# Kernel tuning notes

Hardware: AMD Instinct MI355X
Metric: run time of the kernel (lower is better)

Reference implementation:

```python
import math
import jax, jax.numpy as jnp
import numpy as np

NUM_BUCKETS = 32
MAX_DISTANCE = 128
N_HEADS = 16
D_KV = 64


def _relative_position_bucket(relative_position, num_buckets=NUM_BUCKETS, max_distance=MAX_DISTANCE):
    # bidirectional (encoder) version, faithful to T5Attention._relative_position_bucket
    nb = num_buckets // 2
    rel_buckets = (relative_position > 0).astype(jnp.int32) * nb
    rp = jnp.abs(relative_position)
    max_exact = nb // 2
    is_small = rp < max_exact
    # log-spaced buckets for large distances; clamp arg of log to >=1 to avoid -inf
    rp_large = max_exact + (
        jnp.log(jnp.maximum(rp, 1).astype(jnp.float32) / max_exact)
        / math.log(max_distance / max_exact)
        * (nb - max_exact)
    ).astype(jnp.int32)
    rp_large = jnp.minimum(rp_large, nb - 1)
    return rel_buckets + jnp.where(is_small, rp, rp_large)


def setup_inputs() -> dict:
    key = jax.random.key(0)
    ks = jax.random.split(key, 6)
    B, S, D = 2, 2048, 1024
    scale = 0.02
    return {
        "hidden_states": jax.random.normal(ks[0], (B, S, D), dtype=jnp.float32),
        "Wq": jax.random.normal(ks[1], (D, N_HEADS * D_KV), dtype=jnp.float32) * scale,
        "Wk": jax.random.normal(ks[2], (D, N_HEADS * D_KV), dtype=jnp.float32) * scale,
        "Wv": jax.random.normal(ks[3], (D, N_HEADS * D_KV), dtype=jnp.float32) * scale,
        "Wo": jax.random.normal(ks[4], (N_HEADS * D_KV, D), dtype=jnp.float32) * scale,
        "rel_bias": jax.random.normal(ks[5], (NUM_BUCKETS, N_HEADS), dtype=jnp.float32),
    }


def reference(hidden_states, Wq, Wk, Wv, Wo, rel_bias):
    B, S, D = hidden_states.shape
    H, dk = N_HEADS, D_KV
    q = (hidden_states @ Wq).reshape(B, S, H, dk)
    k = (hidden_states @ Wk).reshape(B, S, H, dk)
    v = (hidden_states @ Wv).reshape(B, S, H, dk)

    pos = jnp.arange(S)
    relative_position = pos[None, :] - pos[:, None]          # [S_q, S_k]
    buckets = _relative_position_bucket(relative_position)    # [S_q, S_k]
    bias = rel_bias[buckets].transpose(2, 0, 1)               # [H, S_q, S_k]

    # T5 attention: NO 1/sqrt(d) scaling
    scores = jnp.einsum('bqhd,bkhd->bhqk', q, k) + bias[None]
    attn = jax.nn.softmax(scores, axis=-1)
    ctx = jnp.einsum('bhqk,bkhd->bqhd', attn, v).reshape(B, S, H * dk)
    return ctx @ Wo
```

## Files before the change

kernel.cpp:

```cpp
#include <hip/hip_runtime.h>
#include <hip/hip_bf16.h>
#include <stdint.h>

#define S_LEN 2048
#define NH 16
#define NB_DELTA (2*S_LEN-1)
#define PST 72
#define LOG2E 1.4426950408889634f

typedef __attribute__((ext_vector_type(8))) __bf16 bf16x8;
typedef __attribute__((ext_vector_type(4))) float f32x4;

__device__ __forceinline__ unsigned short f2bf(float f){
    union { float f; unsigned int u; } v; v.f = f;
    unsigned int u = v.u;
    return (unsigned short)((u + 0x7FFFu + ((u >> 16) & 1u)) >> 16);
}
__device__ __forceinline__ float bf2f(unsigned short u){
    union { unsigned int u; float f; } v; v.u = ((unsigned int)u) << 16;
    return v.f;
}
__device__ __forceinline__ unsigned int pkbf(float a, float b){
    __hip_bfloat162 h = __float22bfloat162_rn(float2{a, b});
    unsigned int u;
    __builtin_memcpy(&u, &h, 4);
    return u;
}
#if __has_builtin(__builtin_amdgcn_exp2f)
__device__ __forceinline__ float fexp2(float x){ return __builtin_amdgcn_exp2f(x); }
#else
__device__ __forceinline__ float fexp2(float x){ return __expf(x * 0.69314718056f); }
#endif

__device__ __forceinline__ void gload16(const void* g, void* l){
    __builtin_amdgcn_global_load_lds(
        (const __attribute__((address_space(1))) void*)(uintptr_t)g,
        (__attribute__((address_space(3))) void*)(uintptr_t)l, 16, 0, 0);
}

__global__ __launch_bounds__(256) void prep_kernel(
    const float* __restrict__ hs, unsigned short* __restrict__ hsb,
    const float* __restrict__ W0, const float* __restrict__ W1,
    const float* __restrict__ W2, const float* __restrict__ W3,
    unsigned short* __restrict__ D0, unsigned short* __restrict__ D1,
    unsigned short* __restrict__ D2, unsigned short* __restrict__ D3,
    const float* __restrict__ rel_bias, float* __restrict__ biasT){
    if (blockIdx.z == 4) {
        int bi = blockIdx.y * 32 + blockIdx.x;
        for (int it = 0; it < 4; it++) {
            int i = bi * 4096 + it * 1024 + threadIdx.x * 4;
            float4 f = *(const float4*)(hs + i);
            ushort4 o;
            o.x = f2bf(f.x); o.y = f2bf(f.y); o.z = f2bf(f.z); o.w = f2bf(f.w);
            *(ushort4*)(hsb + i) = o;
        }
        if (bi < 16) {
            int t = bi * 256 + threadIdx.x;
            if (t < NB_DELTA) {
                int delta = t - (S_LEN - 1);
                int bucket = (delta > 0) ? 16 : 0;
                int a = delta < 0 ? -delta : delta;
                int b;
                if (a < 8) b = a;
                else {
                    int bl = 33 - __builtin_clz(a * a);
                    b = bl < 15 ? bl : 15;
                }
                bucket += b;
                for (int h = 0; h < NH; h++)
                    biasT[h * NB_DELTA + t] = rel_bias[bucket * NH + h];
            }
        }
        return;
    }
    const float* src; unsigned short* dst;
    switch (blockIdx.z) {
        case 0: src = W0; dst = D0; break;
        case 1: src = W1; dst = D1; break;
        case 2: src = W2; dst = D2; break;
        default: src = W3; dst = D3; break;
    }
    __shared__ float tile[32][33];
    int bx = blockIdx.x, by = blockIdx.y;
    int tx = threadIdx.x & 31, ty = threadIdx.x >> 5;
    for (int i = 0; i < 4; i++)
        tile[ty + 8*i][tx] = src[(size_t)(by*32 + ty + 8*i) * 1024 + bx*32 + tx];
    __syncthreads();
    for (int i = 0; i < 4; i++)
        dst[(size_t)(bx*32 + ty + 8*i) * 1024 + by*32 + tx] = f2bf(tile[tx][ty + 8*i]);
}

template<int MODE, int BM>
__global__ __launch_bounds__(256) void gemm_bt_kernel(const unsigned short* __restrict__ A,
                                                      const unsigned short* __restrict__ BT,
                                                      float* __restrict__ C0,
                                                      unsigned short* __restrict__ C1,
                                                      int Kdim, int ldc){
    constexpr int IT = BM / 32;
    __shared__ __align__(16) unsigned short As[BM * 64];
    __shared__ __align__(16) unsigned short Bs[128 * 64];
    const int t = threadIdx.x;
    const int wave = t >> 6, lane = t & 63;
    const int quad = lane >> 4, l16 = lane & 15;
    const int wm = (wave >> 1) * (BM / 2), wn = (wave & 1) * 64;
    const size_t row0 = (size_t)blockIdx.y * BM, col0 = (size_t)blockIdx.x * 128;

    const int srow8 = lane >> 3;
    const int gg = (lane & 7) ^ srow8;
    const unsigned short* gA = A  + (row0 + wave * 8 + srow8) * (size_t)Kdim + gg * 8;
    const unsigned short* gB = BT + (col0 + wave * 8 + srow8) * (size_t)Kdim + gg * 8;

    f32x4 acc[IT][4] = {};

    for (int kt = 0; kt < Kdim; kt += 64) {
        for (int p = 0; p < BM / 32; p++)
            gload16(gA + (size_t)(p * 32) * Kdim + kt, &As[(p * 32 + wave * 8) * 64]);
        for (int p = 0; p < 4; p++)
            gload16(gB + (size_t)(p * 32) * Kdim + kt, &Bs[(p * 32 + wave * 8) * 64]);
        __syncthreads();
        bf16x8 a[2][IT], b[2][4];
        for (int ks = 0; ks < 2; ks++) {
            for (int i = 0; i < IT; i++)
                a[ks][i] = *(const bf16x8*)(&As[(wm + i*16 + l16) * 64 + (((ks*4 + quad) ^ (l16 & 7)) * 8)]);
            for (int j = 0; j < 4; j++)
                b[ks][j] = *(const bf16x8*)(&Bs[(wn + j*16 + l16) * 64 + (((ks*4 + quad) ^ (l16 & 7)) * 8)]);
        }
        for (int ks = 0; ks < 2; ks++)
            for (int i = 0; i < IT; i++)
                for (int j = 0; j < 4; j++)
                    acc[i][j] = __builtin_amdgcn_mfma_f32_16x16x32_bf16(a[ks][i], b[ks][j], acc[i][j], 0, 0, 0);
        __syncthreads();
    }
    for (int i = 0; i < IT; i++)
        for (int j = 0; j < 4; j++) {
            size_t r0 = row0 + wm + i*16 + quad*4;
            size_t c  = col0 + wn + j*16 + l16;
            if (MODE == 0) {
                for (int r = 0; r < 4; r++)
                    C0[(r0 + r) * ldc + c] = acc[i][j][r];
            } else {
                float qs = (c < 1024) ? LOG2E : 1.0f;
                for (int r = 0; r < 4; r++)
                    C1[(r0 + r) * ldc + c] = f2bf(acc[i][j][r] * qs);
            }
        }
}

__global__ __launch_bounds__(256) void vtrans_kernel(const unsigned short* __restrict__ qkv,
                                                     unsigned short* __restrict__ vt){
    __shared__ unsigned short tile[64][72];
    const int v0 = blockIdx.x * 64, s0 = blockIdx.y * 64, b = blockIdx.z;
    const int tx = threadIdx.x & 7, ty = threadIdx.x >> 3;
    for (int i = 0; i < 2; i++)
        *(int4*)&tile[ty + 32*i][tx * 8] =
            *(const int4*)(qkv + (size_t)(b * 2048 + s0 + ty + 32*i) * 3072 + 2048 + v0 + tx * 8);
    __syncthreads();
    for (int i = 0; i < 2; i++) {
        int v = ty + 32*i;
        int sl = tx * 8;
        ushort4 o0, o1;
        o0.x = tile[sl+0][v]; o0.y = tile[sl+1][v]; o0.z = tile[sl+2][v]; o0.w = tile[sl+3][v];
        o1.x = tile[sl+4][v]; o1.y = tile[sl+5][v]; o1.z = tile[sl+6][v]; o1.w = tile[sl+7][v];
        unsigned short* dst = vt + (size_t)(b * 1024 + v0 + v) * 2048 + s0 + sl;
        *(ushort4*)dst = o0; *(ushort4*)(dst + 4) = o1;
    }
}

__global__ __launch_bounds__(256, 4) void flash10_kernel(
    const unsigned short* __restrict__ qkv,
    const unsigned short* __restrict__ vt,
    const float* __restrict__ biasT,
    const float* __restrict__ rel_bias,
    unsigned short* __restrict__ ctxpb,
    float* __restrict__ rsbuf)
{
    const int qt = blockIdx.x, h = blockIdx.y;
    const int b = blockIdx.z >> 1, ck = blockIdx.z & 1;
    const int kt0 = ck << 10;
    const int t = threadIdx.x;
    const int w = t >> 6, lane = t & 63, quad = lane >> 4, l16 = lane & 15;
    const int q0 = qt * 128;

    __shared__ __align__(16) unsigned short Ks[64 * 64];
    __shared__ __align__(16) unsigned short Vs[64 * 64];
    __shared__ __align__(16) unsigned short Pb[128 * PST];
    __shared__ float bias_s[192];

    const float b15 = (rel_bias[15 * NH + h] - 16.f) * LOG2E;
    const float b31 = (rel_bias[31 * NH + h] - 16.f) * LOG2E;

    for (int s = 0; s < 4; s++) {
        int g = t + s * 256;
        int r = g >> 3, c = (g & 7) * 8;
        *(int4*)&Pb[r * PST + c] =
            *(const int4*)(qkv + (size_t)(b * S_LEN + q0 + r) * 3072 + h * 64 + c);
    }
    __syncthreads();
    bf16x8 qb[2][2];
    for (int nt = 0; nt < 2; nt++)
        for (int ks = 0; ks < 2; ks++)
            qb[ks][nt] = *(const bf16x8*)&Pb[(w * 32 + nt * 16 + l16) * PST + ks * 32 + quad * 8];

    float rsum[2] = {0.f, 0.f};
    f32x4 ctx[4][2] = {};

    const float* biasRow = biasT + h * NB_DELTA + 2047;

    const int srow8 = lane >> 3;
    const int gg = (lane & 7) ^ srow8;
    const int swz = ((l16 & 7) * 8);

    for (int kt = kt0; kt < kt0 + 1024; kt += 64) {
        const int off = kt - q0;
        const bool cst = (off >= 255) || (off <= -191);
        __syncthreads();
        {
            const unsigned short* kb = qkv + (size_t)(b * S_LEN + kt + w * 8 + srow8) * 3072 + 1024 + h * 64 + gg * 8;
            const unsigned short* vb = vt + (size_t)(b * 1024 + h * 64 + w * 8 + srow8) * 2048 + kt + gg * 8;
            gload16(kb,                     &Ks[(w * 8) * 64]);
            gload16(kb + (size_t)32 * 3072, &Ks[(32 + w * 8) * 64]);
            gload16(vb,                     &Vs[(w * 8) * 64]);
            gload16(vb + (size_t)32 * 2048, &Vs[(32 + w * 8) * 64]);
            if (!cst && t < 192) bias_s[t] = (biasRow[off - 127 + t] - 16.f) * LOG2E;
        }
        __syncthreads();

        f32x4 st[4][2] = {};
        for (int ks = 0; ks < 2; ks++)
            for (int nb = 0; nb < 4; nb++) {
                bf16x8 ka = *(const bf16x8*)&Ks[(nb * 16 + l16) * 64 + (((ks * 4 + quad) * 8) ^ swz)];
                st[nb][0] = __builtin_amdgcn_mfma_f32_16x16x32_bf16(ka, qb[ks][0], st[nb][0], 0, 0, 0);
                st[nb][1] = __builtin_amdgcn_mfma_f32_16x16x32_bf16(ka, qb[ks][1], st[nb][1], 0, 0, 0);
            }
        const float bc = (off > 0) ? b31 : b15;
        for (int nt = 0; nt < 2; nt++) {
            const int ib = quad * 4 + 127 - w * 32 - nt * 16 - l16;
            float rs = 0.f;
            for (int nb = 0; nb < 4; nb++) {
                float e0, e1, e2, e3;
                if (cst) {
                    e0 = fexp2(st[nb][nt][0] + bc);
                    e1 = fexp2(st[nb][nt][1] + bc);
                    e2 = fexp2(st[nb][nt][2] + bc);
                    e3 = fexp2(st[nb][nt][3] + bc);
                } else {
                    e0 = fexp2(st[nb][nt][0] + bias_s[ib + nb * 16 + 0]);
                    e1 = fexp2(st[nb][nt][1] + bias_s[ib + nb * 16 + 1]);
                    e2 = fexp2(st[nb][nt][2] + bias_s[ib + nb * 16 + 2]);
                    e3 = fexp2(st[nb][nt][3] + bias_s[ib + nb * 16 + 3]);
                }
                rs += (e0 + e1) + (e2 + e3);
                uint2 pk; pk.x = pkbf(e0, e1); pk.y = pkbf(e2, e3);
                *(uint2*)&Pb[(w * 32 + nt * 16 + l16) * PST + nb * 16 + quad * 4] = pk;
            }
            rsum[nt] += rs;
        }
        for (int ks = 0; ks < 2; ks++) {
            bf16x8 pb0 = *(const bf16x8*)&Pb[(w * 32 + l16) * PST + ks * 32 + quad * 8];
            bf16x8 pb1 = *(const bf16x8*)&Pb[(w * 32 + 16 + l16) * PST + ks * 32 + quad * 8];
            for (int nd = 0; nd < 4; nd++) {
                bf16x8 va = *(const bf16x8*)&Vs[(nd * 16 + l16) * 64 + (((ks * 4 + quad) * 8) ^ swz)];
                ctx[nd][0] = __builtin_amdgcn_mfma_f32_16x16x32_bf16(va, pb0, ctx[nd][0], 0, 0, 0);
                ctx[nd][1] = __builtin_amdgcn_mfma_f32_16x16x32_bf16(va, pb1, ctx[nd][1], 0, 0, 0);
            }
        }
    }
    unsigned short* cp = ctxpb + (size_t)ck * 4096 * 1024;
    for (int nt = 0; nt < 2; nt++) {
        float rs = rsum[nt];
        rs += __shfl_xor(rs, 16, 64);
        rs += __shfl_xor(rs, 32, 64);
        int row = b * S_LEN + q0 + w * 32 + nt * 16 + l16;
        if (quad == 0) rsbuf[((size_t)ck * 4096 + row) * 16 + h] = rs;
        for (int nd = 0; nd < 4; nd++) {
            uint2 pk;
            pk.x = pkbf(ctx[nd][nt][0], ctx[nd][nt][1]);
            pk.y = pkbf(ctx[nd][nt][2], ctx[nd][nt][3]);
            *(uint2*)&cp[(size_t)row * 1024 + h * 64 + nd * 16 + quad * 4] = pk;
        }
    }
}

__global__ __launch_bounds__(256) void combine_kernel(const unsigned short* __restrict__ ctxpb,
                                                      const float* __restrict__ rsbuf,
                                                      unsigned short* __restrict__ ctxb){
    int e = blockIdx.x * 256 + threadIdx.x;
    int row = e >> 8;
    int c4 = (e & 255) * 4;
    int h = c4 >> 6;
    float l = rsbuf[(size_t)row * 16 + h] + rsbuf[((size_t)4096 + row) * 16 + h];
    ushort4 a  = *(const ushort4*)&ctxpb[(size_t)row * 1024 + c4];
    ushort4 b2 = *(const ushort4*)&ctxpb[(size_t)4096 * 1024 + (size_t)row * 1024 + c4];
    float inv = 1.f / l;
    uint2 o;
    o.x = pkbf((bf2f(a.x) + bf2f(b2.x)) * inv, (bf2f(a.y) + bf2f(b2.y)) * inv);
    o.y = pkbf((bf2f(a.z) + bf2f(b2.z)) * inv, (bf2f(a.w) + bf2f(b2.w)) * inv);
    *(uint2*)&ctxb[(size_t)row * 1024 + c4] = o;
}

extern "C" void kernel_launch(void* const* d_in, const int* in_sizes, int n_in,
                              void* d_out, int out_size, void* d_ws, size_t ws_size,
                              hipStream_t stream) {
    const float* hs       = (const float*)d_in[0];
    const float* Wq       = (const float*)d_in[1];
    const float* Wk       = (const float*)d_in[2];
    const float* Wv       = (const float*)d_in[3];
    const float* Wo       = (const float*)d_in[4];
    const float* rel_bias = (const float*)d_in[5];
    float* out = (float*)d_out;

    char* ws = (char*)d_ws;
    float* biasT          = (float*)ws;           ws += 262144;
    unsigned short* hsb   = (unsigned short*)ws;  ws += 8388608;
    unsigned short* WT    = (unsigned short*)ws;  ws += 6291456;
    unsigned short* WoT   = (unsigned short*)ws;  ws += 2097152;
    unsigned short* qkvb  = (unsigned short*)ws;  ws += 25165824;
    unsigned short* Vtg   = (unsigned short*)ws;  ws += 8388608;
    unsigned short* ctxb  = (unsigned short*)ws;  ws += 8388608;
    unsigned short* ctxpb = (unsigned short*)ws;  ws += 16777216;
    float* rsbuf          = (float*)ws;

    prep_kernel<<<dim3(32, 32, 5), 256, 0, stream>>>(
        hs, hsb, Wq, Wk, Wv, Wo,
        WT, WT + 1024 * 1024, WT + 2 * 1024 * 1024, WoT, rel_bias, biasT);

    gemm_bt_kernel<1, 64><<<dim3(24, 64), 256, 0, stream>>>(hsb, WT, nullptr, qkvb, 1024, 3072);
    vtrans_kernel<<<dim3(16, 32, 2), 256, 0, stream>>>(qkvb, Vtg);
    flash10_kernel<<<dim3(S_LEN / 128, NH, 4), 256, 0, stream>>>(qkvb, Vtg, biasT, rel_bias, ctxpb, rsbuf);
    combine_kernel<<<4096, 256, 0, stream>>>(ctxpb, rsbuf, ctxb);
    gemm_bt_kernel<0, 64><<<dim3(8, 64), 256, 0, stream>>>(ctxb, WoT, out, nullptr, 1024, 1024);
}
```

Baseline: 203.0 us.

## Fuse V transpose into QKV GEMM epilogue and split-combine into output GEMM

The QKV GEMM now writes Q/K into a narrower buffer and stores V directly transposed, which removes the separate vtrans kernel. The output GEMM loads both split-K partial contexts, normalizes them by the summed row sums and packs bf16 into LDS itself, which removes the combine kernel and the ctxb round trip. This drops two launches and several intermediate buffers. The cost is that the output GEMM's A-tile load becomes synchronous register loads with ALU work in place of async global-to-LDS loads, and the transposed V stores are scattered 8-byte writes.

```diff
diff --git a/kernel.cpp b/kernel.cpp
--- a/kernel.cpp
+++ b/kernel.cpp
@@ -90,84 +90,130 @@
         dst[(size_t)(bx*32 + ty + 8*i) * 1024 + by*32 + tx] = f2bf(tile[tx][ty + 8*i]);
 }
 
-template<int MODE, int BM>
-__global__ __launch_bounds__(256) void gemm_bt_kernel(const unsigned short* __restrict__ A,
-                                                      const unsigned short* __restrict__ BT,
-                                                      float* __restrict__ C0,
-                                                      unsigned short* __restrict__ C1,
-                                                      int Kdim, int ldc){
-    constexpr int IT = BM / 32;
-    __shared__ __align__(16) unsigned short As[BM * 64];
+__global__ __launch_bounds__(256) void gemm_qkv_kernel(const unsigned short* __restrict__ A,
+                                                       const unsigned short* __restrict__ BT,
+                                                       unsigned short* __restrict__ qk,
+                                                       unsigned short* __restrict__ vt){
+    const int Kdim = 1024;
+    __shared__ __align__(16) unsigned short As[64 * 64];
     __shared__ __align__(16) unsigned short Bs[128 * 64];
     const int t = threadIdx.x;
     const int wave = t >> 6, lane = t & 63;
     const int quad = lane >> 4, l16 = lane & 15;
-    const int wm = (wave >> 1) * (BM / 2), wn = (wave & 1) * 64;
-    const size_t row0 = (size_t)blockIdx.y * BM, col0 = (size_t)blockIdx.x * 128;
+    const int wm = (wave >> 1) * 32, wn = (wave & 1) * 64;
+    const size_t row0 = (size_t)blockIdx.y * 64, col0 = (size_t)blockIdx.x * 128;
 
     const int srow8 = lane >> 3;
     const int gg = (lane & 7) ^ srow8;
     const unsigned short* gA = A  + (row0 + wave * 8 + srow8) * (size_t)Kdim + gg * 8;
     const unsigned short* gB = BT + (col0 + wave * 8 + srow8) * (size_t)Kdim + gg * 8;
 
-    f32x4 acc[IT][4] = {};
+    f32x4 acc[2][4] = {};
 
     for (int kt = 0; kt < Kdim; kt += 64) {
-        for (int p = 0; p < BM / 32; p++)
+        for (int p = 0; p < 2; p++)
             gload16(gA + (size_t)(p * 32) * Kdim + kt, &As[(p * 32 + wave * 8) * 64]);
         for (int p = 0; p < 4; p++)
             gload16(gB + (size_t)(p * 32) * Kdim + kt, &Bs[(p * 32 + wave * 8) * 64]);
         __syncthreads();
-        bf16x8 a[2][IT], b[2][4];
+        bf16x8 a[2][2], b[2][4];
         for (int ks = 0; ks < 2; ks++) {
-            for (int i = 0; i < IT; i++)
+            for (int i = 0; i < 2; i++)
                 a[ks][i] = *(const bf16x8*)(&As[(wm + i*16 + l16) * 64 + (((ks*4 + quad) ^ (l16 & 7)) * 8)]);
             for (int j = 0; j < 4; j++)
                 b[ks][j] = *(const bf16x8*)(&Bs[(wn + j*16 + l16) * 64 + (((ks*4 + quad) ^ (l16 & 7)) * 8)]);
         }
         for (int ks = 0; ks < 2; ks++)
-            for (int i = 0; i < IT; i++)
+            for (int i = 0; i < 2; i++)
                 for (int j = 0; j < 4; j++)
                     acc[i][j] = __builtin_amdgcn_mfma_f32_16x16x32_bf16(a[ks][i], b[ks][j], acc[i][j], 0, 0, 0);
         __syncthreads();
     }
-    for (int i = 0; i < IT; i++)
+    for (int i = 0; i < 2; i++)
         for (int j = 0; j < 4; j++) {
             size_t r0 = row0 + wm + i*16 + quad*4;
             size_t c  = col0 + wn + j*16 + l16;
-            if (MODE == 0) {
-                for (int r = 0; r < 4; r++)
-                    C0[(r0 + r) * ldc + c] = acc[i][j][r];
-            } else {
+            if (c < 2048) {
                 float qs = (c < 1024) ? LOG2E : 1.0f;
                 for (int r = 0; r < 4; r++)
-                    C1[(r0 + r) * ldc + c] = f2bf(acc[i][j][r] * qs);
-            }
-        }
-}
-
-__global__ __launch_bounds__(256) void vtrans_kernel(const unsigned short* __restrict__ qkv,
-                                                     unsigned short* __restrict__ vt){
-    __shared__ unsigned short tile[64][72];
-    const int v0 = blockIdx.x * 64, s0 = blockIdx.y * 64, b = blockIdx.z;
-    const int tx = threadIdx.x & 7, ty = threadIdx.x >> 3;
+                    qk[(r0 + r) * 2048 + c] = f2bf(acc[i][j][r] * qs);
+            } else {
+                int bb = (int)(r0 >> 11);
+                int s  = (int)(r0 & 2047);
+                ushort4 pk;
+                pk.x = f2bf(acc[i][j][0]); pk.y = f2bf(acc[i][j][1]);
+                pk.z = f2bf(acc[i][j][2]); pk.w = f2bf(acc[i][j][3]);
+                *(ushort4*)(vt + ((size_t)(bb * 1024) + (c - 2048)) * 2048 + s) = pk;
+            }
+        }
+}
+
+__global__ __launch_bounds__(256) void gemm_out_kernel(const unsigned short* __restrict__ ctxpb,
+                                                       const float* __restrict__ rsbuf,
+                                                       const unsigned short* __restrict__ BT,
+                                                       float* __restrict__ C0){
+    const int Kdim = 1024;
+    __shared__ __align__(16) unsigned short As[64 * 64];
+    __shared__ __align__(16) unsigned short Bs[128 * 64];
+    const int t = threadIdx.x;
+    const int wave = t >> 6, lane = t & 63;
+    const int quad = lane >> 4, l16 = lane & 15;
+    const int wm = (wave >> 1) * 32, wn = (wave & 1) * 64;
+    const size_t row0 = (size_t)blockIdx.y * 64, col0 = (size_t)blockIdx.x * 128;
+
+    const int srow8 = lane >> 3;
+    const int gg = (lane & 7) ^ srow8;
+    const unsigned short* gB = BT + (col0 + wave * 8 + srow8) * (size_t)Kdim + gg * 8;
+    const int arow0 = (int)row0 + wave * 8 + srow8;
+    const int acol  = gg * 8;
+
+    f32x4 acc[2][4] = {};
+
+    for (int kt = 0; kt < Kdim; kt += 64) {
+        for (int p = 0; p < 4; p++)
+            gload16(gB + (size_t)(p * 32) * Kdim + kt, &Bs[(p * 32 + wave * 8) * 64]);
+        const int h = kt >> 6;
+        for (int p = 0; p < 2; p++) {
+            const int r = arow0 + p * 32;
+            uint4 a0 = *(const uint4*)&ctxpb[(size_t)r * 1024 + kt + acol];
+            uint4 a1 = *(const uint4*)&ctxpb[(size_t)4096 * 1024 + (size_t)r * 1024 + kt + acol];
+            float inv = 1.f / (rsbuf[(size_t)r * 16 + h] + rsbuf[((size_t)4096 + r) * 16 + h]);
+            uint4 o;
+            o.x = pkbf((bf2f(a0.x & 0xffff) + bf2f(a1.x & 0xffff)) * inv,
+                       (bf2f(a0.x >> 16)    + bf2f(a1.x >> 16))    * inv);
+            o.y = pkbf((bf2f(a0.y & 0xffff) + bf2f(a1.y & 0xffff)) * inv,
+                       (bf2f(a0.y >> 16)    + bf2f(a1.y >> 16))    * inv);
+            o.z = pkbf((bf2f(a0.z & 0xffff) + bf2f(a1.z & 0xffff)) * inv,
+                       (bf2f(a0.z >> 16)    + bf2f(a1.z >> 16))    * inv);
+            o.w = pkbf((bf2f(a0.w & 0xffff) + bf2f(a1.w & 0xffff)) * inv,
+                       (bf2f(a0.w >> 16)    + bf2f(a1.w >> 16))    * inv);
+            *(uint4*)&As[(p * 32 + wave * 8 + srow8) * 64 + (lane & 7) * 8] = o;
+        }
+        __syncthreads();
+        bf16x8 a[2][2], b[2][4];
+        for (int ks = 0; ks < 2; ks++) {
+            for (int i = 0; i < 2; i++)
+                a[ks][i] = *(const bf16x8*)(&As[(wm + i*16 + l16) * 64 + (((ks*4 + quad) ^ (l16 & 7)) * 8)]);
+            for (int j = 0; j < 4; j++)
+                b[ks][j] = *(const bf16x8*)(&Bs[(wn + j*16 + l16) * 64 + (((ks*4 + quad) ^ (l16 & 7)) * 8)]);
+        }
+        for (int ks = 0; ks < 2; ks++)
+            for (int i = 0; i < 2; i++)
+                for (int j = 0; j < 4; j++)
+                    acc[i][j] = __builtin_amdgcn_mfma_f32_16x16x32_bf16(a[ks][i], b[ks][j], acc[i][j], 0, 0, 0);
+        __syncthreads();
+    }
     for (int i = 0; i < 2; i++)
-        *(int4*)&tile[ty + 32*i][tx * 8] =
-            *(const int4*)(qkv + (size_t)(b * 2048 + s0 + ty + 32*i) * 3072 + 2048 + v0 + tx * 8);
-    __syncthreads();
-    for (int i = 0; i < 2; i++) {
-        int v = ty + 32*i;
-        int sl = tx * 8;
-        ushort4 o0, o1;
-        o0.x = tile[sl+0][v]; o0.y = tile[sl+1][v]; o0.z = tile[sl+2][v]; o0.w = tile[sl+3][v];
-        o1.x = tile[sl+4][v]; o1.y = tile[sl+5][v]; o1.z = tile[sl+6][v]; o1.w = tile[sl+7][v];
-        unsigned short* dst = vt + (size_t)(b * 1024 + v0 + v) * 2048 + s0 + sl;
-        *(ushort4*)dst = o0; *(ushort4*)(dst + 4) = o1;
-    }
+        for (int j = 0; j < 4; j++) {
+            size_t r0 = row0 + wm + i*16 + quad*4;
+            size_t c  = col0 + wn + j*16 + l16;
+            for (int r = 0; r < 4; r++)
+                C0[(r0 + r) * 1024 + c] = acc[i][j][r];
+        }
 }
 
 __global__ __launch_bounds__(256, 4) void flash10_kernel(
-    const unsigned short* __restrict__ qkv,
+    const unsigned short* __restrict__ qk,
     const unsigned short* __restrict__ vt,
     const float* __restrict__ biasT,
     const float* __restrict__ rel_bias,
@@ -193,7 +239,7 @@
         int g = t + s * 256;
         int r = g >> 3, c = (g & 7) * 8;
         *(int4*)&Pb[r * PST + c] =
-            *(const int4*)(qkv + (size_t)(b * S_LEN + q0 + r) * 3072 + h * 64 + c);
+            *(const int4*)(qk + (size_t)(b * S_LEN + q0 + r) * 2048 + h * 64 + c);
     }
     __syncthreads();
     bf16x8 qb[2][2];
@@ -215,10 +261,10 @@
         const bool cst = (off >= 255) || (off <= -191);
         __syncthreads();
         {
-            const unsigned short* kb = qkv + (size_t)(b * S_LEN + kt + w * 8 + srow8) * 3072 + 1024 + h * 64 + gg * 8;
+            const unsigned short* kb = qk + (size_t)(b * S_LEN + kt + w * 8 + srow8) * 2048 + 1024 + h * 64 + gg * 8;
             const unsigned short* vb = vt + (size_t)(b * 1024 + h * 64 + w * 8 + srow8) * 2048 + kt + gg * 8;
             gload16(kb,                     &Ks[(w * 8) * 64]);
-            gload16(kb + (size_t)32 * 3072, &Ks[(32 + w * 8) * 64]);
+            gload16(kb + (size_t)32 * 2048, &Ks[(32 + w * 8) * 64]);
             gload16(vb,                     &Vs[(w * 8) * 64]);
             gload16(vb + (size_t)32 * 2048, &Vs[(32 + w * 8) * 64]);
             if (!cst && t < 192) bias_s[t] = (biasRow[off - 127 + t] - 16.f) * LOG2E;
@@ -281,23 +327,6 @@
     }
 }
 
-__global__ __launch_bounds__(256) void combine_kernel(const unsigned short* __restrict__ ctxpb,
-                                                      const float* __restrict__ rsbuf,
-                                                      unsigned short* __restrict__ ctxb){
-    int e = blockIdx.x * 256 + threadIdx.x;
-    int row = e >> 8;
-    int c4 = (e & 255) * 4;
-    int h = c4 >> 6;
-    float l = rsbuf[(size_t)row * 16 + h] + rsbuf[((size_t)4096 + row) * 16 + h];
-    ushort4 a  = *(const ushort4*)&ctxpb[(size_t)row * 1024 + c4];
-    ushort4 b2 = *(const ushort4*)&ctxpb[(size_t)4096 * 1024 + (size_t)row * 1024 + c4];
-    float inv = 1.f / l;
-    uint2 o;
-    o.x = pkbf((bf2f(a.x) + bf2f(b2.x)) * inv, (bf2f(a.y) + bf2f(b2.y)) * inv);
-    o.y = pkbf((bf2f(a.z) + bf2f(b2.z)) * inv, (bf2f(a.w) + bf2f(b2.w)) * inv);
-    *(uint2*)&ctxb[(size_t)row * 1024 + c4] = o;
-}
-
 extern "C" void kernel_launch(void* const* d_in, const int* in_sizes, int n_in,
                               void* d_out, int out_size, void* d_ws, size_t ws_size,
                               hipStream_t stream) {
@@ -314,9 +343,8 @@
     unsigned short* hsb   = (unsigned short*)ws;  ws += 8388608;
     unsigned short* WT    = (unsigned short*)ws;  ws += 6291456;
     unsigned short* WoT   = (unsigned short*)ws;  ws += 2097152;
-    unsigned short* qkvb  = (unsigned short*)ws;  ws += 25165824;
+    unsigned short* qkbuf = (unsigned short*)ws;  ws += 16777216;
     unsigned short* Vtg   = (unsigned short*)ws;  ws += 8388608;
-    unsigned short* ctxb  = (unsigned short*)ws;  ws += 8388608;
     unsigned short* ctxpb = (unsigned short*)ws;  ws += 16777216;
     float* rsbuf          = (float*)ws;
 
@@ -324,9 +352,7 @@
         hs, hsb, Wq, Wk, Wv, Wo,
         WT, WT + 1024 * 1024, WT + 2 * 1024 * 1024, WoT, rel_bias, biasT);
 
-    gemm_bt_kernel<1, 64><<<dim3(24, 64), 256, 0, stream>>>(hsb, WT, nullptr, qkvb, 1024, 3072);
-    vtrans_kernel<<<dim3(16, 32, 2), 256, 0, stream>>>(qkvb, Vtg);
-    flash10_kernel<<<dim3(S_LEN / 128, NH, 4), 256, 0, stream>>>(qkvb, Vtg, biasT, rel_bias, ctxpb, rsbuf);
-    combine_kernel<<<4096, 256, 0, stream>>>(ctxpb, rsbuf, ctxb);
-    gemm_bt_kernel<0, 64><<<dim3(8, 64), 256, 0, stream>>>(ctxb, WoT, out, nullptr, 1024, 1024);
-}
+    gemm_qkv_kernel<<<dim3(24, 64), 256, 0, stream>>>(hsb, WT, qkbuf, Vtg);
+    flash10_kernel<<<dim3(S_LEN / 128, NH, 4), 256, 0, stream>>>(qkbuf, Vtg, biasT, rel_bias, ctxpb, rsbuf);
+    gemm_out_kernel<<<dim3(8, 64), 256, 0, stream>>>(ctxpb, rsbuf, WoT, out);
+}
```

After: 203.2 us. No clear change (+0.1%).
